# Kernel optimization log

Measured on AMD Instinct MI355X. Metric: run time of the kernel, lower is better.

## Reference

```python
import jax, jax.numpy as jnp
import numpy as np

N, E, D, H = 50000, 800000, 128, 8
HD = D // H  # 16
HID = 512
EPS = 1e-5
SLOPE = 0.2  # DGL GATConv default negative_slope


def setup_inputs() -> dict:
    key = jax.random.key(0)
    ks = jax.random.split(key, 10)
    s = 0.1
    return {
        "x": jax.random.normal(ks[0], (N, D), jnp.float32),
        "src": jax.random.randint(ks[1], (E,), 0, N),
        "dst": jax.random.randint(ks[2], (E,), 0, N),
        "W": jax.random.normal(ks[3], (D, D), jnp.float32) * s,
        "attn_l": jax.random.normal(ks[4], (H, HD), jnp.float32) * s,
        "attn_r": jax.random.normal(ks[5], (H, HD), jnp.float32) * s,
        "bias_gat": jnp.zeros((D,), jnp.float32),
        "bn1_gamma": jnp.ones((D,), jnp.float32),
        "bn1_beta": jnp.zeros((D,), jnp.float32),
        "W1": jax.random.normal(ks[6], (D, HID), jnp.float32) * s,
        "b1": jnp.zeros((HID,), jnp.float32),
        "W2": jax.random.normal(ks[7], (HID, D), jnp.float32) * s,
        "b2": jnp.zeros((D,), jnp.float32),
        "bn2_gamma": jnp.ones((D,), jnp.float32),
        "bn2_beta": jnp.zeros((D,), jnp.float32),
    }


def _batchnorm(v, gamma, beta):
    # BatchNorm1d, training-mode forward (batch statistics, biased var)
    mu = v.mean(0)
    var = v.var(0)
    return (v - mu) * jax.lax.rsqrt(var + EPS) * gamma + beta


def reference(x, src, dst, W, attn_l, attn_r, bias_gat,
              bn1_gamma, bn1_beta, W1, b1, W2, b2, bn2_gamma, bn2_beta):
    n = x.shape[0]
    # GATConv: project + per-head attention logits
    feat = (x @ W).reshape(n, H, HD)                     # [N, H, hd]
    el = jnp.einsum('nhd,hd->nh', feat, attn_l)          # [N, H]
    er = jnp.einsum('nhd,hd->nh', feat, attn_r)          # [N, H]
    e = el[src] + er[dst]                                # [E, H]
    e = jnp.where(e > 0, e, SLOPE * e)                   # LeakyReLU
    # segment (edge) softmax over incoming edges of each dst node
    m = jax.ops.segment_max(e, dst, num_segments=n)      # [N, H]
    ee = jnp.exp(e - m[dst])
    denom = jax.ops.segment_sum(ee, dst, num_segments=n)
    alpha = ee / denom[dst]                              # [E, H]
    # weighted scatter-aggregate of source features
    msg = feat[src] * alpha[:, :, None]                  # [E, H, hd]
    agg = jax.ops.segment_sum(msg, dst, num_segments=n)  # [N, H, hd]
    h = agg.reshape(n, D) + bias_gat
    # BN -> Linear -> ReLU -> Linear -> BN
    h = _batchnorm(h, bn1_gamma, bn1_beta)
    h = jax.nn.relu(h @ W1 + b1) @ W2 + b2
    h = _batchnorm(h, bn2_gamma, bn2_beta)
    return h
```

## Files before the change

kernel.cpp:

```cpp
#include <hip/hip_runtime.h>
#include <math.h>

#define NHEAD 8
#define DD 128
#define HIDD 512
#define NB 768

typedef _Float16 half8 __attribute__((ext_vector_type(8)));
typedef _Float16 half4 __attribute__((ext_vector_type(4)));
typedef float floatx4 __attribute__((ext_vector_type(4)));

__device__ __forceinline__ int swz256(int row, int bytecol) {
  return row * 256 + (bytecol ^ ((row & 15) << 4));
}

__global__ __launch_bounds__(256) void pack_kernel(
    const float* __restrict__ W, const float* __restrict__ W1,
    const float* __restrict__ W2, _Float16* __restrict__ WP,
    _Float16* __restrict__ W1TP, _Float16* __restrict__ W2P)
{
  int i = blockIdx.x * 256 + threadIdx.x;
  if (i < 4 * 128 * 4 * 8) {
    int ii = i & 7, l4 = (i >> 3) & 3, col = (i >> 5) & 127, kc = i >> 12;
    WP[i] = (_Float16)W[(kc * 32 + l4 * 8 + ii) * DD + col];
  }
  if (i < 65536) {
    int ii = i & 7, e = (i >> 3) & 63, tile = i >> 9;
    int l4 = e >> 4, l15 = e & 15, hb = tile >> 2, kc = tile & 3;
    W1TP[i] = (_Float16)W1[(size_t)(kc * 32 + l4 * 8 + ii) * HIDD + hb * 16 + l15];
  }
  if (i < 65536) {
    int ii = i & 7, e = (i >> 3) & 63, tile = i >> 9;
    int l4 = e >> 4, l15 = e & 15, c = tile >> 3, cb = tile & 7;
    int hidden = (ii < 4) ? (2 * c) * 16 + 4 * l4 + ii
                          : (2 * c + 1) * 16 + 4 * l4 + (ii - 4);
    W2P[i] = (_Float16)W2[(size_t)hidden * DD + cb * 16 + l15];
  }
}

__global__ __launch_bounds__(256) void feat_mfma_kernel(
    const float* __restrict__ x, const _Float16* __restrict__ WP,
    _Float16* __restrict__ feat16, int N, int T)
{
  __shared__ char xs[32 * 256];
  const int tid = threadIdx.x;
  const int wv = tid >> 6, lane = tid & 63;
  const int l15 = lane & 15, l4 = lane >> 4;
  const int row = tid >> 3, seg = tid & 7;

  int t = blockIdx.x;
  float4 pre[4];
  {
    const int n = t * 32 + row;
    const bool ok = (t < T) && (n < N);
    const float4* sp = (const float4*)(x + (size_t)n * DD + seg * 16);
    const float4 z = make_float4(0.f, 0.f, 0.f, 0.f);
    #pragma unroll
    for (int c = 0; c < 4; ++c) pre[c] = ok ? sp[c] : z;
  }

  for (; t < T; t += NB) {
    const int n0 = t * 32;
    {
      half8 h0, h1;
      #pragma unroll
      for (int c = 0; c < 4; ++c) {
        float4 v = pre[c];
        if (c < 2) {
          h0[c * 4 + 0] = (_Float16)v.x; h0[c * 4 + 1] = (_Float16)v.y;
          h0[c * 4 + 2] = (_Float16)v.z; h0[c * 4 + 3] = (_Float16)v.w;
        } else {
          h1[(c - 2) * 4 + 0] = (_Float16)v.x; h1[(c - 2) * 4 + 1] = (_Float16)v.y;
          h1[(c - 2) * 4 + 2] = (_Float16)v.z; h1[(c - 2) * 4 + 3] = (_Float16)v.w;
        }
      }
      *(half8*)(xs + swz256(row, seg * 32)) = h0;
      *(half8*)(xs + swz256(row, seg * 32 + 16)) = h1;
    }
    __syncthreads();

    floatx4 acc[2][2];
    #pragma unroll
    for (int mf = 0; mf < 2; ++mf) { acc[mf][0] = (floatx4)0.f; acc[mf][1] = (floatx4)0.f; }

    #pragma unroll
    for (int kc = 0; kc < 4; ++kc) {
      half8 b0 = *(const half8*)(WP + ((kc * 128 + wv * 32 + l15) * 4 + l4) * 8);
      half8 b1 = *(const half8*)(WP + ((kc * 128 + wv * 32 + 16 + l15) * 4 + l4) * 8);
      #pragma unroll
      for (int mf = 0; mf < 2; ++mf) {
        half8 af = *(const half8*)(xs + swz256(mf * 16 + l15, kc * 64 + l4 * 16));
        acc[mf][0] = __builtin_amdgcn_mfma_f32_16x16x32_f16(af, b0, acc[mf][0], 0, 0, 0);
        acc[mf][1] = __builtin_amdgcn_mfma_f32_16x16x32_f16(af, b1, acc[mf][1], 0, 0, 0);
      }
    }

    {
      const int tn = t + NB;
      const int n = tn * 32 + row;
      const bool ok = (tn < T) && (n < N);
      const float4* sp = (const float4*)(x + (size_t)n * DD + seg * 16);
      const float4 z = make_float4(0.f, 0.f, 0.f, 0.f);
      #pragma unroll
      for (int c = 0; c < 4; ++c) pre[c] = ok ? sp[c] : z;
    }

    #pragma unroll
    for (int mf = 0; mf < 2; ++mf) {
      #pragma unroll
      for (int r = 0; r < 4; ++r) {
        const int rown = n0 + mf * 16 + l4 * 4 + r;
        if (rown < N) {
          feat16[(size_t)rown * DD + wv * 32 + l15] = (_Float16)acc[mf][0][r];
          feat16[(size_t)rown * DD + wv * 32 + 16 + l15] = (_Float16)acc[mf][1][r];
        }
      }
    }
    __syncthreads();
  }
}

__global__ __launch_bounds__(256) void elr_kernel(
    const _Float16* __restrict__ feat16, const float* __restrict__ attn_l,
    const float* __restrict__ attn_r, float* __restrict__ el,
    float* __restrict__ er, int N)
{
  int gid = blockIdx.x * 256 + threadIdx.x;
  if (gid >= N * NHEAD) return;
  const int n = gid >> 3, h = gid & 7;
  const half8* fp = (const half8*)(feat16 + (size_t)n * DD + h * 16);
  half8 f0 = fp[0], f1 = fp[1];
  float sl = 0.f, sr = 0.f;
  #pragma unroll
  for (int d = 0; d < 8; ++d) {
    float v0 = (float)f0[d], v1 = (float)f1[d];
    sl = fmaf(v0, attn_l[h * 16 + d], sl);
    sl = fmaf(v1, attn_l[h * 16 + 8 + d], sl);
    sr = fmaf(v0, attn_r[h * 16 + d], sr);
    sr = fmaf(v1, attn_r[h * 16 + 8 + d], sr);
  }
  el[gid] = sl;
  er[gid] = sr;
}

__global__ __launch_bounds__(256) void count_kernel(const int* __restrict__ dst,
                                                    int* __restrict__ counts,
                                                    int* __restrict__ rank, int E)
{
  int e = blockIdx.x * 256 + threadIdx.x;
  if (e < E) rank[e] = atomicAdd(&counts[dst[e]], 1);
}

__global__ __launch_bounds__(256) void scan1_kernel(const int* __restrict__ counts,
                                                    int* __restrict__ offsets,
                                                    int* __restrict__ btot)
{
  __shared__ int wsum[4];
  const int lane = threadIdx.x & 63;
  const int wid = threadIdx.x >> 6;
  int4 c = *(const int4*)(counts + blockIdx.x * 1024 + threadIdx.x * 4);
  int q = c.x + c.y + c.z + c.w;
  int incl = q;
  #pragma unroll
  for (int d = 1; d < 64; d <<= 1) {
    int t = __shfl_up(incl, d, 64);
    if (lane >= d) incl += t;
  }
  if (lane == 63) wsum[wid] = incl;
  __syncthreads();
  int wprefix = 0;
  for (int w = 0; w < wid; ++w) wprefix += wsum[w];
  int excl = wprefix + incl - q;
  int4 o;
  o.x = excl; o.y = excl + c.x; o.z = o.y + c.y; o.w = o.z + c.z;
  *(int4*)(offsets + blockIdx.x * 1024 + threadIdx.x * 4) = o;
  if (threadIdx.x == 0) btot[blockIdx.x] = wsum[0] + wsum[1] + wsum[2] + wsum[3];
}

__global__ __launch_bounds__(64) void scan2_kernel(const int* __restrict__ btot,
                                                   int* __restrict__ bof, int nchunk)
{
  const int t = threadIdx.x;
  const int K = (nchunk + 63) >> 6;
  const int base = t * K;
  int s = 0;
  for (int i = 0; i < K; ++i) if (base + i < nchunk) s += btot[base + i];
  int incl = s;
  #pragma unroll
  for (int d = 1; d < 64; d <<= 1) {
    int tt = __shfl_up(incl, d, 64);
    if (t >= d) incl += tt;
  }
  int run = incl - s;
  for (int i = 0; i < K; ++i) if (base + i < nchunk) { bof[base + i] = run; run += btot[base + i]; }
}

__global__ __launch_bounds__(256) void fill_kernel(const int* __restrict__ src,
                                                   const int* __restrict__ dst,
                                                   const int* __restrict__ offsets,
                                                   const int* __restrict__ bof,
                                                   const int* __restrict__ rank,
                                                   int* __restrict__ srcl, int E)
{
  int e = blockIdx.x * 256 + threadIdx.x;
  if (e < E) {
    int d = dst[e];
    srcl[offsets[d] + bof[d >> 10] + rank[e]] = src[e];
  }
}

__global__ __launch_bounds__(256) void agg_kernel(
    const _Float16* __restrict__ feat16, const float* __restrict__ el,
    const float* __restrict__ er, const int* __restrict__ offsets,
    const int* __restrict__ bof, const int* __restrict__ srcl,
    const float* __restrict__ bias, float* __restrict__ hout, int N)
{
  int gid = blockIdx.x * 256 + threadIdx.x;
  if (gid >= N * 16) return;
  const int n = gid >> 4;
  const int sub = gid & 15;
  const int hh = sub >> 1;
  const int half = sub & 1;
  const int o0 = offsets[n] + bof[n >> 10];
  const int o1 = offsets[n + 1] + bof[(n + 1) >> 10];
  const int cnt = o1 - o0;
  const int mid = o0 + ((cnt + 1) >> 1);
  int j = half ? mid : o0;
  const int je = half ? o1 : mid;
  const float er_nh = er[n * NHEAD + hh];

  float s = 0.f;
  float a[16];
  #pragma unroll
  for (int d = 0; d < 16; ++d) a[d] = 0.f;

  for (; j + 3 < je; j += 4) {
    const int s0 = srcl[j], s1 = srcl[j + 1], s2 = srcl[j + 2], s3 = srcl[j + 3];
    float e0 = el[s0 * NHEAD + hh] + er_nh;
    float e1 = el[s1 * NHEAD + hh] + er_nh;
    float e2 = el[s2 * NHEAD + hh] + er_nh;
    float e3 = el[s3 * NHEAD + hh] + er_nh;
    const half8* f0p = (const half8*)(feat16 + (size_t)s0 * DD + hh * 16);
    const half8* f1p = (const half8*)(feat16 + (size_t)s1 * DD + hh * 16);
    const half8* f2p = (const half8*)(feat16 + (size_t)s2 * DD + hh * 16);
    const half8* f3p = (const half8*)(feat16 + (size_t)s3 * DD + hh * 16);
    e0 = e0 > 0.f ? e0 : 0.2f * e0;
    e1 = e1 > 0.f ? e1 : 0.2f * e1;
    e2 = e2 > 0.f ? e2 : 0.2f * e2;
    e3 = e3 > 0.f ? e3 : 0.2f * e3;
    const float p0 = __expf(e0), p1 = __expf(e1), p2 = __expf(e2), p3 = __expf(e3);
    half8 f00 = f0p[0], f01 = f0p[1];
    half8 f10 = f1p[0], f11 = f1p[1];
    half8 f20 = f2p[0], f21 = f2p[1];
    half8 f30 = f3p[0], f31 = f3p[1];
    s += (p0 + p1) + (p2 + p3);
    #pragma unroll
    for (int d = 0; d < 8; ++d) {
      float t0 = fmaf(p0, (float)f00[d], fmaf(p1, (float)f10[d], a[d]));
      a[d] = fmaf(p2, (float)f20[d], fmaf(p3, (float)f30[d], t0));
      float t1 = fmaf(p0, (float)f01[d], fmaf(p1, (float)f11[d], a[d + 8]));
      a[d + 8] = fmaf(p2, (float)f21[d], fmaf(p3, (float)f31[d], t1));
    }
  }
  for (; j < je; ++j) {
    const int s0 = srcl[j];
    float e0 = el[s0 * NHEAD + hh] + er_nh;
    e0 = e0 > 0.f ? e0 : 0.2f * e0;
    const float p0 = __expf(e0);
    const half8* f0p = (const half8*)(feat16 + (size_t)s0 * DD + hh * 16);
    half8 f00 = f0p[0], f01 = f0p[1];
    s += p0;
    #pragma unroll
    for (int d = 0; d < 8; ++d) {
      a[d]     = fmaf(p0, (float)f00[d], a[d]);
      a[d + 8] = fmaf(p0, (float)f01[d], a[d + 8]);
    }
  }

  s += __shfl_xor(s, 1, 64);
  #pragma unroll
  for (int d = 0; d < 16; ++d) a[d] += __shfl_xor(a[d], 1, 64);

  const float inv = (cnt > 0) ? 1.f / s : 0.f;
  const int cbase = hh * 16 + half * 8;
  float* op = hout + (size_t)n * DD + cbase;
  const float* bp = bias + cbase;
  const int abase = half * 8;
  float4 o0v, o1v;
  o0v.x = fmaf(a[abase + 0], inv, bp[0]);
  o0v.y = fmaf(a[abase + 1], inv, bp[1]);
  o0v.z = fmaf(a[abase + 2], inv, bp[2]);
  o0v.w = fmaf(a[abase + 3], inv, bp[3]);
  o1v.x = fmaf(a[abase + 4], inv, bp[4]);
  o1v.y = fmaf(a[abase + 5], inv, bp[5]);
  o1v.z = fmaf(a[abase + 6], inv, bp[6]);
  o1v.w = fmaf(a[abase + 7], inv, bp[7]);
  *(float4*)(op) = o0v;
  *(float4*)(op + 4) = o1v;
}

__global__ __launch_bounds__(256) void bnstats_kernel(
    const float* __restrict__ h, float* __restrict__ sums,
    float* __restrict__ sumsq, int N)
{
  __shared__ float rs[256], rss[256];
  const int c = threadIdx.x & 127;
  const int half = threadIdx.x >> 7;
  const int rowsPer = (N + gridDim.x - 1) / gridDim.x;
  const int r0 = blockIdx.x * rowsPer;
  const int r1 = min(N, r0 + rowsPer);
  float s = 0.f, ss = 0.f;
  for (int r = r0 + half; r < r1; r += 2) {
    float v = h[(size_t)r * DD + c];
    s += v; ss += v * v;
  }
  rs[threadIdx.x] = s; rss[threadIdx.x] = ss;
  __syncthreads();
  if (threadIdx.x < 128) {
    s = rs[threadIdx.x] + rs[threadIdx.x + 128];
    ss = rss[threadIdx.x] + rss[threadIdx.x + 128];
    atomicAdd(&sums[c], s);
    atomicAdd(&sumsq[c], ss);
  }
}

__global__ __launch_bounds__(256, 2) void mlp_mfma_kernel(
    const float* __restrict__ hbuf, const float* __restrict__ sum1,
    const float* __restrict__ ss1, const float* __restrict__ bn1_g,
    const float* __restrict__ bn1_b, const _Float16* __restrict__ W1TP,
    const _Float16* __restrict__ W2P, const float* __restrict__ b1,
    const float* __restrict__ b2, float* __restrict__ out, int N)
{
  __shared__ char myA[8192];
  __shared__ char xch[3 * 8192];
  const int tid = threadIdx.x;
  const int wv = tid >> 6;
  const int lane = tid & 63;
  const int l15 = lane & 15, l4 = lane >> 4;
  const int n0 = blockIdx.x * 32;
  if (n0 >= N) return;

  {
    const int c0 = (tid & 31) * 4;
    const int rq = tid >> 5;
    float sc[4], sh[4];
    #pragma unroll
    for (int jj = 0; jj < 4; ++jj) {
      float mean = sum1[c0 + jj] / (float)N;
      float var = ss1[c0 + jj] / (float)N - mean * mean;
      float s = bn1_g[c0 + jj] * rsqrtf(var + 1e-5f);
      sc[jj] = s; sh[jj] = bn1_b[c0 + jj] - mean * s;
    }
    #pragma unroll
    for (int it = 0; it < 4; ++it) {
      const int row = it * 8 + rq;
      const int n = n0 + row;
      float4 v = make_float4(0.f, 0.f, 0.f, 0.f);
      if (n < N) v = *(const float4*)(hbuf + (size_t)n * DD + c0);
      half4 hv;
      hv[0] = (_Float16)fmaf(v.x, sc[0], sh[0]);
      hv[1] = (_Float16)fmaf(v.y, sc[1], sh[1]);
      hv[2] = (_Float16)fmaf(v.z, sc[2], sh[2]);
      hv[3] = (_Float16)fmaf(v.w, sc[3], sh[3]);
      *(half4*)(myA + swz256(row, c0 * 2)) = hv;
    }
  }
  __syncthreads();

  half8 xf[2][4];
  #pragma unroll
  for (int nb = 0; nb < 2; ++nb)
    #pragma unroll
    for (int kc = 0; kc < 4; ++kc)
      xf[nb][kc] = *(const half8*)(myA + swz256(nb * 16 + l15, kc * 64 + l4 * 16));

  floatx4 acc2[2][8];
  #pragma unroll
  for (int nb = 0; nb < 2; ++nb)
    #pragma unroll
    for (int cb = 0; cb < 8; ++cb) acc2[nb][cb] = (floatx4)0.f;

  half8 a2s[4][2];
  #pragma unroll
  for (int c8 = 0; c8 < 4; ++c8) {
    const int c = wv * 4 + c8;
    floatx4 dA[2], dB[2];
    dA[0] = (floatx4)0.f; dA[1] = (floatx4)0.f;
    dB[0] = (floatx4)0.f; dB[1] = (floatx4)0.f;
    half8 wA[4], wB[4];
    #pragma unroll
    for (int kc = 0; kc < 4; ++kc) {
      wA[kc] = *(const half8*)(W1TP + (size_t)((2 * c) * 4 + kc) * 512 + (l4 * 16 + l15) * 8);
      wB[kc] = *(const half8*)(W1TP + (size_t)((2 * c + 1) * 4 + kc) * 512 + (l4 * 16 + l15) * 8);
    }
    __builtin_amdgcn_s_setprio(1);
    #pragma unroll
    for (int kc = 0; kc < 4; ++kc) {
      dA[0] = __builtin_amdgcn_mfma_f32_16x16x32_f16(wA[kc], xf[0][kc], dA[0], 0, 0, 0);
      dA[1] = __builtin_amdgcn_mfma_f32_16x16x32_f16(wA[kc], xf[1][kc], dA[1], 0, 0, 0);
      dB[0] = __builtin_amdgcn_mfma_f32_16x16x32_f16(wB[kc], xf[0][kc], dB[0], 0, 0, 0);
      dB[1] = __builtin_amdgcn_mfma_f32_16x16x32_f16(wB[kc], xf[1][kc], dB[1], 0, 0, 0);
    }
    __builtin_amdgcn_s_setprio(0);
    floatx4 bA = *(const floatx4*)&b1[(2 * c) * 16 + l4 * 4];
    floatx4 bB = *(const floatx4*)&b1[(2 * c + 1) * 16 + l4 * 4];
    #pragma unroll
    for (int nb = 0; nb < 2; ++nb) {
      #pragma unroll
      for (int r = 0; r < 4; ++r) {
        float vA = dA[nb][r] + bA[r];
        float vB = dB[nb][r] + bB[r];
        a2s[c8][nb][r]     = (_Float16)(vA > 0.f ? vA : 0.f);
        a2s[c8][nb][r + 4] = (_Float16)(vB > 0.f ? vB : 0.f);
      }
    }
  }
  #pragma unroll
  for (int c8 = 0; c8 < 4; ++c8) {
    const int c = wv * 4 + c8;
    half8 w2[8];
    #pragma unroll
    for (int cb = 0; cb < 8; ++cb)
      w2[cb] = *(const half8*)(W2P + (size_t)(c * 8 + cb) * 512 + (l4 * 16 + l15) * 8);
    __builtin_amdgcn_s_setprio(1);
    #pragma unroll
    for (int cb = 0; cb < 8; ++cb) {
      acc2[0][cb] = __builtin_amdgcn_mfma_f32_16x16x32_f16(a2s[c8][0], w2[cb], acc2[0][cb], 0, 0, 0);
      acc2[1][cb] = __builtin_amdgcn_mfma_f32_16x16x32_f16(a2s[c8][1], w2[cb], acc2[1][cb], 0, 0, 0);
    }
    __builtin_amdgcn_s_setprio(0);
  }

  if (wv != 0) {
    char* myX = xch + (wv - 1) * 8192;
    #pragma unroll
    for (int nb = 0; nb < 2; ++nb) {
      #pragma unroll
      for (int cb = 0; cb < 8; ++cb) {
        half4 hv;
        #pragma unroll
        for (int r = 0; r < 4; ++r) hv[r] = (_Float16)acc2[nb][cb][r];
        *(half4*)(myX + ((nb * 8 + cb) * 64 + lane) * 8) = hv;
      }
    }
  }
  __syncthreads();
  if (wv == 0) {
    float b2v[8];
    #pragma unroll
    for (int cb = 0; cb < 8; ++cb) b2v[cb] = b2[cb * 16 + l15];
    #pragma unroll
    for (int sw = 0; sw < 3; ++sw) {
      #pragma unroll
      for (int nb = 0; nb < 2; ++nb) {
        #pragma unroll
        for (int cb = 0; cb < 8; ++cb) {
          half4 hv = *(const half4*)(xch + sw * 8192 + ((nb * 8 + cb) * 64 + lane) * 8);
          #pragma unroll
          for (int r = 0; r < 4; ++r) acc2[nb][cb][r] += (float)hv[r];
        }
      }
    }
    #pragma unroll
    for (int nb = 0; nb < 2; ++nb) {
      #pragma unroll
      for (int r = 0; r < 4; ++r) {
        const int rown = n0 + nb * 16 + l4 * 4 + r;
        if (rown < N) {
          #pragma unroll
          for (int cb = 0; cb < 8; ++cb)
            out[(size_t)rown * DD + cb * 16 + l15] = acc2[nb][cb][r] + b2v[cb];
        }
      }
    }
  }
}

__global__ __launch_bounds__(256) void applybn_kernel(
    float* __restrict__ out, const float* __restrict__ sum2,
    const float* __restrict__ ss2, const float* __restrict__ gamma,
    const float* __restrict__ beta, int N, int total4)
{
  __shared__ float sc[128], sh[128];
  if (threadIdx.x < 128) {
    int c = threadIdx.x;
    float mean = sum2[c] / (float)N;
    float var = ss2[c] / (float)N - mean * mean;
    float s = gamma[c] * rsqrtf(var + 1e-5f);
    sc[c] = s;
    sh[c] = beta[c] - mean * s;
  }
  __syncthreads();
  int i = blockIdx.x * 256 + threadIdx.x;
  const int stride = gridDim.x * 256;
  for (; i < total4; i += stride) {
    float4 v = ((float4*)out)[i];
    int c = (i & 31) * 4;
    float4 scv = *(const float4*)&sc[c];
    float4 shv = *(const float4*)&sh[c];
    v.x = fmaf(v.x, scv.x, shv.x); v.y = fmaf(v.y, scv.y, shv.y);
    v.z = fmaf(v.z, scv.z, shv.z); v.w = fmaf(v.w, scv.w, shv.w);
    ((float4*)out)[i] = v;
  }
}

extern "C" void kernel_launch(void* const* d_in, const int* in_sizes, int n_in,
                              void* d_out, int out_size, void* d_ws, size_t ws_size,
                              hipStream_t stream) {
  const float* x        = (const float*)d_in[0];
  const int*   src      = (const int*)d_in[1];
  const int*   dst      = (const int*)d_in[2];
  const float* W        = (const float*)d_in[3];
  const float* attn_l   = (const float*)d_in[4];
  const float* attn_r   = (const float*)d_in[5];
  const float* bias_gat = (const float*)d_in[6];
  const float* bn1_g    = (const float*)d_in[7];
  const float* bn1_b    = (const float*)d_in[8];
  const float* W1       = (const float*)d_in[9];
  const float* b1       = (const float*)d_in[10];
  const float* W2       = (const float*)d_in[11];
  const float* b2       = (const float*)d_in[12];
  const float* bn2_g    = (const float*)d_in[13];
  const float* bn2_b    = (const float*)d_in[14];
  float* out = (float*)d_out;

  const int N = in_sizes[0] / DD;
  const int E = in_sizes[1];
  const int NPAD = ((N + 1023) / 1024) * 1024;
  const int NCHUNK = NPAD / 1024;
  const int T = (N + 31) / 32;

  _Float16* feat16 = (_Float16*)d_ws;
  float* hbuf = (float*)(feat16 + (size_t)((N + 1) & ~1) * DD);
  float* el   = hbuf + (size_t)N * DD;
  float* er   = el + (size_t)N * NHEAD;
  int* counts = (int*)(er + (size_t)N * NHEAD);
  int* offsets = counts + NPAD;
  int* srcl   = offsets + NPAD;
  int* btot   = srcl + E;
  int* bof    = btot + 64;
  float* stats = (float*)(bof + 64);
  float* sum1 = stats, *ss1 = stats + 128;
  float* sum2 = stats + 256, *ss2 = stats + 384;
  _Float16* WP   = (_Float16*)(stats + 1024);
  _Float16* W1TP = WP + 4 * 128 * 32;
  _Float16* W2P  = W1TP + 65536;
  int* rank = (int*)hbuf;

  hipMemsetAsync(counts, 0, (size_t)NPAD * sizeof(int), stream);
  hipMemsetAsync(stats, 0, 512 * sizeof(float), stream);

  pack_kernel<<<256, 256, 0, stream>>>(W, W1, W2, WP, W1TP, W2P);
  feat_mfma_kernel<<<NB, 256, 0, stream>>>(x, WP, feat16, N, T);
  elr_kernel<<<(N * NHEAD + 255) / 256, 256, 0, stream>>>(feat16, attn_l, attn_r, el, er, N);
  count_kernel<<<(E + 255) / 256, 256, 0, stream>>>(dst, counts, rank, E);
  scan1_kernel<<<NCHUNK, 256, 0, stream>>>(counts, offsets, btot);
  scan2_kernel<<<1, 64, 0, stream>>>(btot, bof, NCHUNK);
  fill_kernel<<<(E + 255) / 256, 256, 0, stream>>>(src, dst, offsets, bof, rank, srcl, E);
  agg_kernel<<<(N * 16 + 255) / 256, 256, 0, stream>>>(feat16, el, er, offsets, bof,
                                                       srcl, bias_gat, hbuf, N);
  bnstats_kernel<<<256, 256, 0, stream>>>(hbuf, sum1, ss1, N);
  mlp_mfma_kernel<<<T, 256, 0, stream>>>(hbuf, sum1, ss1, bn1_g, bn1_b, W1TP, W2P,
                                         b1, b2, out, N);
  bnstats_kernel<<<256, 256, 0, stream>>>(out, sum2, ss2, N);
  applybn_kernel<<<2048, 256, 0, stream>>>(out, sum2, ss2, bn2_g, bn2_b, N, N * DD / 4);
}
```

Measured before the change: 224.5 us.

## Fuse attention logits, edge counting and MLP weight packing into feature GEMM launch

Computes el/er inside the feature GEMM epilogue with lane shuffles, which removes the separate elr kernel and its re-read of feat16. The dst counting and W1/W2 packing run as extra block ranges of the same launch, so they can overlap the GEMM instead of running as separate kernels. Second-BN column statistics are now accumulated in the MLP epilogue with shuffles and atomics, which drops one full pass over the output. In exchange el/er are taken from fp32 accumulators rather than fp16-rounded features, which changes numerics slightly, and the MLP kernel issues more atomics.

```diff
diff --git a/kernel.cpp b/kernel.cpp
--- a/kernel.cpp
+++ b/kernel.cpp
@@ -15,38 +15,54 @@
 }
 
 __global__ __launch_bounds__(256) void pack_kernel(
-    const float* __restrict__ W, const float* __restrict__ W1,
-    const float* __restrict__ W2, _Float16* __restrict__ WP,
-    _Float16* __restrict__ W1TP, _Float16* __restrict__ W2P)
+    const float* __restrict__ W, _Float16* __restrict__ WP)
 {
   int i = blockIdx.x * 256 + threadIdx.x;
   if (i < 4 * 128 * 4 * 8) {
     int ii = i & 7, l4 = (i >> 3) & 3, col = (i >> 5) & 127, kc = i >> 12;
     WP[i] = (_Float16)W[(kc * 32 + l4 * 8 + ii) * DD + col];
   }
-  if (i < 65536) {
-    int ii = i & 7, e = (i >> 3) & 63, tile = i >> 9;
-    int l4 = e >> 4, l15 = e & 15, hb = tile >> 2, kc = tile & 3;
-    W1TP[i] = (_Float16)W1[(size_t)(kc * 32 + l4 * 8 + ii) * HIDD + hb * 16 + l15];
-  }
-  if (i < 65536) {
-    int ii = i & 7, e = (i >> 3) & 63, tile = i >> 9;
-    int l4 = e >> 4, l15 = e & 15, c = tile >> 3, cb = tile & 7;
-    int hidden = (ii < 4) ? (2 * c) * 16 + 4 * l4 + ii
-                          : (2 * c + 1) * 16 + 4 * l4 + (ii - 4);
-    W2P[i] = (_Float16)W2[(size_t)hidden * DD + cb * 16 + l15];
-  }
-}
-
-__global__ __launch_bounds__(256) void feat_mfma_kernel(
+}
+
+__global__ __launch_bounds__(256) void featcount_kernel(
     const float* __restrict__ x, const _Float16* __restrict__ WP,
-    _Float16* __restrict__ feat16, int N, int T)
-{
+    const float* __restrict__ attn_l, const float* __restrict__ attn_r,
+    _Float16* __restrict__ feat16, float* __restrict__ el, float* __restrict__ er,
+    int N, int T,
+    const int* __restrict__ dst, int* __restrict__ counts,
+    int* __restrict__ rank, int E,
+    const float* __restrict__ W1, const float* __restrict__ W2,
+    _Float16* __restrict__ W1TP, _Float16* __restrict__ W2P, int countB)
+{
+  if (blockIdx.x >= NB + countB) {
+    int i = (blockIdx.x - NB - countB) * 256 + threadIdx.x;
+    {
+      int ii = i & 7, e = (i >> 3) & 63, tile = i >> 9;
+      int l4 = e >> 4, l15 = e & 15, hb = tile >> 2, kc = tile & 3;
+      W1TP[i] = (_Float16)W1[(size_t)(kc * 32 + l4 * 8 + ii) * HIDD + hb * 16 + l15];
+    }
+    {
+      int ii = i & 7, e = (i >> 3) & 63, tile = i >> 9;
+      int l4 = e >> 4, l15 = e & 15, c = tile >> 3, cb = tile & 7;
+      int hidden = (ii < 4) ? (2 * c) * 16 + 4 * l4 + ii
+                            : (2 * c + 1) * 16 + 4 * l4 + (ii - 4);
+      W2P[i] = (_Float16)W2[(size_t)hidden * DD + cb * 16 + l15];
+    }
+    return;
+  }
+  if (blockIdx.x >= NB) {
+    int e = (blockIdx.x - NB) * 256 + threadIdx.x;
+    if (e < E) rank[e] = atomicAdd(&counts[dst[e]], 1);
+    return;
+  }
   __shared__ char xs[32 * 256];
   const int tid = threadIdx.x;
   const int wv = tid >> 6, lane = tid & 63;
   const int l15 = lane & 15, l4 = lane >> 4;
   const int row = tid >> 3, seg = tid & 7;
+
+  const float al0 = attn_l[wv * 32 + l15], al1 = attn_l[wv * 32 + 16 + l15];
+  const float ar0 = attn_r[wv * 32 + l15], ar1 = attn_r[wv * 32 + 16 + l15];
 
   int t = blockIdx.x;
   float4 pre[4];
@@ -110,45 +126,26 @@
       #pragma unroll
       for (int r = 0; r < 4; ++r) {
         const int rown = n0 + mf * 16 + l4 * 4 + r;
+        float v0 = acc[mf][0][r], v1 = acc[mf][1][r];
+        float e0l = v0 * al0, e0r = v0 * ar0;
+        float e1l = v1 * al1, e1r = v1 * ar1;
+        #pragma unroll
+        for (int d = 1; d < 16; d <<= 1) {
+          e0l += __shfl_xor(e0l, d, 64); e0r += __shfl_xor(e0r, d, 64);
+          e1l += __shfl_xor(e1l, d, 64); e1r += __shfl_xor(e1r, d, 64);
+        }
         if (rown < N) {
-          feat16[(size_t)rown * DD + wv * 32 + l15] = (_Float16)acc[mf][0][r];
-          feat16[(size_t)rown * DD + wv * 32 + 16 + l15] = (_Float16)acc[mf][1][r];
+          feat16[(size_t)rown * DD + wv * 32 + l15] = (_Float16)v0;
+          feat16[(size_t)rown * DD + wv * 32 + 16 + l15] = (_Float16)v1;
+          if (l15 == 0) {
+            el[rown * NHEAD + wv * 2] = e0l;     er[rown * NHEAD + wv * 2] = e0r;
+            el[rown * NHEAD + wv * 2 + 1] = e1l; er[rown * NHEAD + wv * 2 + 1] = e1r;
+          }
         }
       }
     }
     __syncthreads();
   }
-}
-
-__global__ __launch_bounds__(256) void elr_kernel(
-    const _Float16* __restrict__ feat16, const float* __restrict__ attn_l,
-    const float* __restrict__ attn_r, float* __restrict__ el,
-    float* __restrict__ er, int N)
-{
-  int gid = blockIdx.x * 256 + threadIdx.x;
-  if (gid >= N * NHEAD) return;
-  const int n = gid >> 3, h = gid & 7;
-  const half8* fp = (const half8*)(feat16 + (size_t)n * DD + h * 16);
-  half8 f0 = fp[0], f1 = fp[1];
-  float sl = 0.f, sr = 0.f;
-  #pragma unroll
-  for (int d = 0; d < 8; ++d) {
-    float v0 = (float)f0[d], v1 = (float)f1[d];
-    sl = fmaf(v0, attn_l[h * 16 + d], sl);
-    sl = fmaf(v1, attn_l[h * 16 + 8 + d], sl);
-    sr = fmaf(v0, attn_r[h * 16 + d], sr);
-    sr = fmaf(v1, attn_r[h * 16 + 8 + d], sr);
-  }
-  el[gid] = sl;
-  er[gid] = sr;
-}
-
-__global__ __launch_bounds__(256) void count_kernel(const int* __restrict__ dst,
-                                                    int* __restrict__ counts,
-                                                    int* __restrict__ rank, int E)
-{
-  int e = blockIdx.x * 256 + threadIdx.x;
-  if (e < E) rank[e] = atomicAdd(&counts[dst[e]], 1);
 }
 
 __global__ __launch_bounds__(256) void scan1_kernel(const int* __restrict__ counts,
@@ -329,7 +326,8 @@
     const float* __restrict__ ss1, const float* __restrict__ bn1_g,
     const float* __restrict__ bn1_b, const _Float16* __restrict__ W1TP,
     const _Float16* __restrict__ W2P, const float* __restrict__ b1,
-    const float* __restrict__ b2, float* __restrict__ out, int N)
+    const float* __restrict__ b2, float* __restrict__ out,
+    float* __restrict__ sums2, float* __restrict__ sumsq2, int N)
 {
   __shared__ char myA[8192];
   __shared__ char xch[3 * 8192];
@@ -461,16 +459,36 @@
         }
       }
     }
+    float scol[8], sqcol[8];
+    #pragma unroll
+    for (int cb = 0; cb < 8; ++cb) { scol[cb] = 0.f; sqcol[cb] = 0.f; }
     #pragma unroll
     for (int nb = 0; nb < 2; ++nb) {
       #pragma unroll
       for (int r = 0; r < 4; ++r) {
         const int rown = n0 + nb * 16 + l4 * 4 + r;
-        if (rown < N) {
-          #pragma unroll
-          for (int cb = 0; cb < 8; ++cb)
-            out[(size_t)rown * DD + cb * 16 + l15] = acc2[nb][cb][r] + b2v[cb];
+        const bool ok = rown < N;
+        #pragma unroll
+        for (int cb = 0; cb < 8; ++cb) {
+          float v = ok ? (acc2[nb][cb][r] + b2v[cb]) : 0.f;
+          if (ok) out[(size_t)rown * DD + cb * 16 + l15] = v;
+          scol[cb] += v;
+          sqcol[cb] += v * v;
         }
+      }
+    }
+    #pragma unroll
+    for (int cb = 0; cb < 8; ++cb) {
+      scol[cb] += __shfl_xor(scol[cb], 16, 64);
+      scol[cb] += __shfl_xor(scol[cb], 32, 64);
+      sqcol[cb] += __shfl_xor(sqcol[cb], 16, 64);
+      sqcol[cb] += __shfl_xor(sqcol[cb], 32, 64);
+    }
+    if (l4 == 0) {
+      #pragma unroll
+      for (int cb = 0; cb < 8; ++cb) {
+        atomicAdd(&sums2[cb * 16 + l15], scol[cb]);
+        atomicAdd(&sumsq2[cb * 16 + l15], sqcol[cb]);
       }
     }
   }
@@ -529,6 +547,7 @@
   const int NPAD = ((N + 1023) / 1024) * 1024;
   const int NCHUNK = NPAD / 1024;
   const int T = (N + 31) / 32;
+  const int countB = (E + 255) / 256;
 
   _Float16* feat16 = (_Float16*)d_ws;
   float* hbuf = (float*)(feat16 + (size_t)((N + 1) & ~1) * DD);
@@ -550,18 +569,17 @@
   hipMemsetAsync(counts, 0, (size_t)NPAD * sizeof(int), stream);
   hipMemsetAsync(stats, 0, 512 * sizeof(float), stream);
 
-  pack_kernel<<<256, 256, 0, stream>>>(W, W1, W2, WP, W1TP, W2P);
-  feat_mfma_kernel<<<NB, 256, 0, stream>>>(x, WP, feat16, N, T);
-  elr_kernel<<<(N * NHEAD + 255) / 256, 256, 0, stream>>>(feat16, attn_l, attn_r, el, er, N);
-  count_kernel<<<(E + 255) / 256, 256, 0, stream>>>(dst, counts, rank, E);
+  pack_kernel<<<64, 256, 0, stream>>>(W, WP);
+  featcount_kernel<<<NB + countB + 256, 256, 0, stream>>>(
+      x, WP, attn_l, attn_r, feat16, el, er, N, T,
+      dst, counts, rank, E, W1, W2, W1TP, W2P, countB);
   scan1_kernel<<<NCHUNK, 256, 0, stream>>>(counts, offsets, btot);
   scan2_kernel<<<1, 64, 0, stream>>>(btot, bof, NCHUNK);
-  fill_kernel<<<(E + 255) / 256, 256, 0, stream>>>(src, dst, offsets, bof, rank, srcl, E);
+  fill_kernel<<<countB, 256, 0, stream>>>(src, dst, offsets, bof, rank, srcl, E);
   agg_kernel<<<(N * 16 + 255) / 256, 256, 0, stream>>>(feat16, el, er, offsets, bof,
                                                        srcl, bias_gat, hbuf, N);
   bnstats_kernel<<<256, 256, 0, stream>>>(hbuf, sum1, ss1, N);
   mlp_mfma_kernel<<<T, 256, 0, stream>>>(hbuf, sum1, ss1, bn1_g, bn1_b, W1TP, W2P,
-                                         b1, b2, out, N);
-  bnstats_kernel<<<256, 256, 0, stream>>>(out, sum2, ss2, N);
+                                         b1, b2, out, sum2, ss2, N);
   applybn_kernel<<<2048, 256, 0, stream>>>(out, sum2, ss2, bn2_g, bn2_b, N, N * DD / 4);
 }
```

Result: faster. 206.6 us, median of 2 (-8.0%).
